# Kernel optimization log

Measured on AMD Instinct MI355X. Metric: run time of the kernel, lower is better.

The kernel has to match this reference:

```python
import jax, jax.numpy as jnp
import numpy as np

B, S, D, H, F = 8, 1024, 1024, 16, 4096
DH = D // H  # 64
EPS = 1e-5


def layer_norm(x, g, b):
    mu = jnp.mean(x, axis=-1, keepdims=True)
    var = jnp.mean(jnp.square(x - mu), axis=-1, keepdims=True)
    return (x - mu) * jax.lax.rsqrt(var + EPS) * g + b


def mha(q_in, k_in, v_in, wq, wk, wv, wo, causal):
    # wq/wk/wv: [H, D, DH] (stacked per-head nn.Linear weights, pre-transposed)
    Q = jnp.einsum('bsd,hdk->bhsk', q_in, wq)
    K = jnp.einsum('bsd,hdk->bhsk', k_in, wk)
    V = jnp.einsum('bsd,hdk->bhsk', v_in, wv)
    scores = jnp.einsum('bhsk,bhtk->bhst', Q, K) / jnp.sqrt(jnp.asarray(DH, Q.dtype))
    if causal:
        mask = jnp.triu(jnp.ones((S, S), dtype=bool), k=1)  # True = inaccessible
        scores = jnp.where(mask, -jnp.inf, scores)
    A = jax.nn.softmax(scores, axis=-1)
    heads = jnp.einsum('bhst,bhtk->bhsk', A, V)
    heads = heads.transpose(0, 2, 1, 3).reshape(q_in.shape[0], q_in.shape[1], D)
    return heads @ wo.T  # nn.Linear convention


def setup_inputs() -> dict:
    key = jax.random.key(0)
    ks = jax.random.split(key, 16)
    sc = 1.0 / np.sqrt(D)
    scf = 1.0 / np.sqrt(F)
    return {
        'embeds': jax.random.normal(ks[0], (B, S, D), jnp.float32),
        'encoder_output': jax.random.normal(ks[1], (B, S, D), jnp.float32),
        'wq1': jax.random.normal(ks[2], (H, D, DH), jnp.float32) * sc,
        'wk1': jax.random.normal(ks[3], (H, D, DH), jnp.float32) * sc,
        'wv1': jax.random.normal(ks[4], (H, D, DH), jnp.float32) * sc,
        'wo1': jax.random.normal(ks[5], (D, D), jnp.float32) * sc,
        'wq2': jax.random.normal(ks[6], (H, D, DH), jnp.float32) * sc,
        'wk2': jax.random.normal(ks[7], (H, D, DH), jnp.float32) * sc,
        'wv2': jax.random.normal(ks[8], (H, D, DH), jnp.float32) * sc,
        'wo2': jax.random.normal(ks[9], (D, D), jnp.float32) * sc,
        'ln1_g': jnp.ones((D,), jnp.float32), 'ln1_b': jnp.zeros((D,), jnp.float32),
        'ln2_g': jnp.ones((D,), jnp.float32), 'ln2_b': jnp.zeros((D,), jnp.float32),
        'ln3_g': jnp.ones((D,), jnp.float32), 'ln3_b': jnp.zeros((D,), jnp.float32),
        'w1': jax.random.normal(ks[10], (F, D), jnp.float32) * sc,
        'b1': jnp.zeros((F,), jnp.float32),
        'w2': jax.random.normal(ks[11], (D, F), jnp.float32) * scf,
        'b2': jnp.zeros((D,), jnp.float32),
    }


def reference(embeds, encoder_output, wq1, wk1, wv1, wo1, wq2, wk2, wv2, wo2,
              ln1_g, ln1_b, ln2_g, ln2_b, ln3_g, ln3_b, w1, b1, w2, b2):
    # masked (causal) self-attention + residual + LN
    sa = mha(embeds, embeds, embeds, wq1, wk1, wv1, wo1, causal=True)
    x1 = layer_norm(sa + embeds, ln1_g, ln1_b)
    # cross-attention (no mask) + residual + LN
    ca = mha(x1, encoder_output, encoder_output, wq2, wk2, wv2, wo2, causal=False)
    x2 = layer_norm(ca + x1, ln2_g, ln2_b)
    # feedforward (Linear -> GELU(exact) -> Linear) + residual + LN
    ff = jax.nn.gelu(x2 @ w1.T + b1, approximate=False) @ w2.T + b2
    return layer_norm(ff + x2, ln3_g, ln3_b)
```

## Files before the change

kernel.cpp:

```cpp
#include <hip/hip_runtime.h>
#include <cstdint>
#include <cstddef>

typedef unsigned short u16;
typedef __attribute__((ext_vector_type(4))) float f32x4;
typedef __attribute__((ext_vector_type(4))) float f4;
typedef __attribute__((ext_vector_type(8))) short short8x;
typedef __attribute__((ext_vector_type(4))) u16 u16x4;
typedef __attribute__((ext_vector_type(8))) u16 u16x8;

#define DEV static __device__ __forceinline__

DEV void gl_lds16(const void* g, void* l) {
  __builtin_amdgcn_global_load_lds(
      (const __attribute__((address_space(1))) unsigned int*)g,
      (__attribute__((address_space(3))) unsigned int*)l, 16, 0, 0);
}

DEV u16 f2bf(float f) {
  unsigned u = __float_as_uint(f);
  u += 0x7fffu + ((u >> 16) & 1u);
  return (u16)(u >> 16);
}


__global__ __launch_bounds__(256) void cast_bf16_2(const float* __restrict__ X0, const float* __restrict__ X1,
                                                   u16* __restrict__ Y0, u16* __restrict__ Y1) {
  const float* X = blockIdx.y ? X1 : X0;
  u16* Y = blockIdx.y ? Y1 : Y0;
  size_t i = ((size_t)blockIdx.x * 256 + threadIdx.x) * 4;
  f4 v = *(const f4*)(X + i);
  u16x4 y;
#pragma unroll
  for (int j = 0; j < 4; ++j) y[j] = f2bf(v[j]);
  *(u16x4*)(Y + i) = y;
}

__global__ __launch_bounds__(256) void cast_wqkv6(const float* __restrict__ W0, const float* __restrict__ W1,
                                                  const float* __restrict__ W2, const float* __restrict__ W3,
                                                  const float* __restrict__ W4, const float* __restrict__ W5,
                                                  u16* __restrict__ Wbase) {
  __shared__ float tile[64][65];
  const int t = threadIdx.x;
  const int h = blockIdx.y;
  const int z = blockIdx.z;
  const int d0 = blockIdx.x * 64;
  const float* W = (z == 0) ? W0 : (z == 1) ? W1 : (z == 2) ? W2 : (z == 3) ? W3 : (z == 4) ? W4 : W5;
  u16* Wt = Wbase + (size_t)z * (1024 * 1024);
  const float* Wb = W + (size_t)h * (1024 * 64);
  const int di = t >> 2;
  const int j0 = (t & 3) * 16;
#pragma unroll
  for (int c = 0; c < 4; ++c) {
    f4 v = *(const f4*)(Wb + (size_t)(d0 + di) * 64 + j0 + c * 4);
#pragma unroll
    for (int j = 0; j < 4; ++j) tile[di][j0 + c * 4 + j] = v[j];
  }
  __syncthreads();
  const int k = t >> 2;
  const int dd0 = (t & 3) * 16;
  u16x8 o0, o1;
#pragma unroll
  for (int u = 0; u < 8; ++u) o0[u] = f2bf(tile[dd0 + u][k]);
#pragma unroll
  for (int u = 0; u < 8; ++u) o1[u] = f2bf(tile[dd0 + 8 + u][k]);
  u16* dst = Wt + (size_t)(h * 64 + k) * 1024 + d0 + dd0;
  *(u16x8*)(dst) = o0;
  *(u16x8*)(dst + 8) = o1;
}

__global__ __launch_bounds__(256) void transpose_v(const u16* __restrict__ V, u16* __restrict__ Vt,
                                                   int vstride, int voff) {
  __shared__ u16 tile[32][72];
  const int t = threadIdx.x;
  const int bh = blockIdx.y;
  const int s0 = blockIdx.x * 32;
  const u16* Vb = V + (size_t)(bh >> 4) * (1024 * (size_t)vstride) + voff + (bh & 15) * 64;
  const int si = t >> 3, d0 = (t & 7) * 8;
  u16x8 val = *(const u16x8*)(Vb + (size_t)(s0 + si) * vstride + d0);
#pragma unroll
  for (int u = 0; u < 8; ++u) tile[si][d0 + u] = val[u];
  __syncthreads();
  const int d = t >> 2, sj0 = (t & 3) * 8;
  u16x8 o;
#pragma unroll
  for (int u = 0; u < 8; ++u) o[u] = tile[sj0 + u][d];
  *(u16x8*)(Vt + (size_t)bh * (64 * 1024) + (size_t)d * 1024 + s0 + sj0) = o;
}

template <int EPI>
__global__ __launch_bounds__(256, 3) void gemm_bt(const u16* __restrict__ A, const u16* __restrict__ Bt,
                                                  void* __restrict__ C, const float* __restrict__ bias,
                                                  int Krow, int Kit, int ldc, long long zC) {
  __shared__ u16 As0[128 * 32], Bs0[128 * 32];
  __shared__ u16 As1[128 * 32], Bs1[128 * 32];
  const int t = threadIdx.x;
  const int wave = t >> 6, lane = t & 63;
  const int lr = lane & 15, lkg = lane >> 4;
  const int swz = (lr >> 1) & 3;
  const int wr = (wave >> 1) * 64, wc = (wave & 1) * 64;

  const int gx = gridDim.x;
  const int nwg = gx * gridDim.y;
  const int flat = blockIdx.y * gx + blockIdx.x;
  const int wg = (flat & 7) * (nwg >> 3) + (flat >> 3);
  const int m0 = (wg / gx) * 128, n0 = (wg % gx) * 128;

  const int schunk = ((t & 3) ^ ((t >> 3) & 3)) << 4;
  const size_t rowb = (size_t)Krow * 2;
  const size_t rowskip = (size_t)64 * rowb;
  const size_t zoff = (size_t)blockIdx.z * (size_t)Kit * 2;
  const char* gA0 = (const char*)A + (size_t)(m0 + (t >> 2)) * rowb + zoff + schunk;
  const char* gA1 = gA0 + rowskip;
  const char* gB0 = (const char*)Bt + (size_t)(n0 + (t >> 2)) * rowb + zoff + schunk;
  const char* gB1 = gB0 + rowskip;

  char* dA0 = (char*)As0 + wave * 1024;
  char* dB0 = (char*)Bs0 + wave * 1024;
  char* dA1 = (char*)As1 + wave * 1024;
  char* dB1 = (char*)Bs1 + wave * 1024;

  const int aoff = (wr + lr) * 64 + ((lkg ^ swz) << 4);
  const int boff = (wc + lr) * 64 + ((lkg ^ swz) << 4);
  const char* rA0 = (const char*)As0 + aoff;
  const char* rB0 = (const char*)Bs0 + boff;
  const char* rA1 = (const char*)As1 + aoff;
  const char* rB1 = (const char*)Bs1 + boff;

  const f32x4 fzero = {0.f, 0.f, 0.f, 0.f};
  f32x4 acc[4][4];
#pragma unroll
  for (int m = 0; m < 4; ++m)
#pragma unroll
    for (int n = 0; n < 4; ++n) acc[m][n] = fzero;

  auto compute = [&](const char* rA, const char* rB) {
    short8x aF[4], bF[4];
#pragma unroll
    for (int m = 0; m < 4; ++m) aF[m] = *(const short8x*)(rA + m * 1024);
#pragma unroll
    for (int n = 0; n < 4; ++n) bF[n] = *(const short8x*)(rB + n * 1024);
#pragma unroll
    for (int m = 0; m < 4; ++m)
#pragma unroll
      for (int n = 0; n < 4; ++n)
        acc[m][n] = __builtin_amdgcn_mfma_f32_16x16x32_bf16(aF[m], bF[n], acc[m][n], 0, 0, 0);
  };

  gl_lds16(gA0, dA0); gl_lds16(gA1, dA0 + 4096);
  gl_lds16(gB0, dB0); gl_lds16(gB1, dB0 + 4096);
  gA0 += 64; gA1 += 64; gB0 += 64; gB1 += 64;
  __syncthreads();

  const int nk2 = Kit >> 6;
  for (int p = 0; p < nk2; ++p) {
    gl_lds16(gA0, dA1); gl_lds16(gA1, dA1 + 4096);
    gl_lds16(gB0, dB1); gl_lds16(gB1, dB1 + 4096);
    gA0 += 64; gA1 += 64; gB0 += 64; gB1 += 64;
    compute(rA0, rB0);
    __syncthreads();
    if (p + 1 < nk2) {
      gl_lds16(gA0, dA0); gl_lds16(gA1, dA0 + 4096);
      gl_lds16(gB0, dB0); gl_lds16(gB1, dB0 + 4096);
    }
    gA0 += 64; gA1 += 64; gB0 += 64; gB1 += 64;
    compute(rA1, rB1);
    __syncthreads();
  }

#pragma unroll
  for (int m = 0; m < 4; ++m) {
#pragma unroll
    for (int rr = 0; rr < 4; ++rr) {
      const int gm = m0 + wr + m * 16 + lkg * 4 + rr;
#pragma unroll
      for (int n = 0; n < 4; ++n) {
        const int gn = n0 + wc + n * 16 + lr;
        float v = acc[m][n][rr];
        if (EPI == 2) v += bias[gn];
        if (EPI == 2) v = 0.5f * v * (1.0f + erff(v * 0.70710678118654752f));
        if (EPI == 4) v *= 0.125f;
        if (EPI == 5 && gn < 1024) v *= 0.125f;
        if (EPI == 1)
          ((float*)C)[(size_t)blockIdx.z * zC + (size_t)gm * ldc + gn] = v;
        else
          ((u16*)C)[(size_t)gm * ldc + gn] = f2bf(v);
      }
    }
  }
}

__global__ __launch_bounds__(256, 3) void gemm_q2kv2(const u16* __restrict__ A1, const u16* __restrict__ B1,
                                                     u16* __restrict__ C1, const u16* __restrict__ A2,
                                                     const u16* __restrict__ B2, u16* __restrict__ C2) {
  __shared__ u16 As0[128 * 32], Bs0[128 * 32];
  __shared__ u16 As1[128 * 32], Bs1[128 * 32];
  const int t = threadIdx.x;
  const int wave = t >> 6, lane = t & 63;
  const int lr = lane & 15, lkg = lane >> 4;
  const int swz = (lr >> 1) & 3;
  const int wr = (wave >> 1) * 64, wc = (wave & 1) * 64;

  const int nwg = 24 * 64;
  const int flat = blockIdx.y * 24 + blockIdx.x;
  const int wg = (flat & 7) * (nwg >> 3) + (flat >> 3);

  const int sub = (wg >= 512);
  const int wl = sub ? (wg - 512) : wg;
  const int gxl = sub ? 16 : 8;
  const int m0 = (wl / gxl) * 128, n0 = (wl % gxl) * 128;
  const u16* A = sub ? A2 : A1;
  const u16* Bt = sub ? B2 : B1;
  u16* C = sub ? C2 : C1;
  const int ldc = sub ? 2048 : 3072;
  const float scale = sub ? 1.0f : 0.125f;

  const int schunk = ((t & 3) ^ ((t >> 3) & 3)) << 4;
  const size_t rowb = 2048;
  const size_t rowskip = (size_t)64 * rowb;
  const char* gA0 = (const char*)A + (size_t)(m0 + (t >> 2)) * rowb + schunk;
  const char* gA1 = gA0 + rowskip;
  const char* gB0 = (const char*)Bt + (size_t)(n0 + (t >> 2)) * rowb + schunk;
  const char* gB1 = gB0 + rowskip;

  char* dA0 = (char*)As0 + wave * 1024;
  char* dB0 = (char*)Bs0 + wave * 1024;
  char* dA1 = (char*)As1 + wave * 1024;
  char* dB1 = (char*)Bs1 + wave * 1024;

  const int aoff = (wr + lr) * 64 + ((lkg ^ swz) << 4);
  const int boff = (wc + lr) * 64 + ((lkg ^ swz) << 4);
  const char* rA0 = (const char*)As0 + aoff;
  const char* rB0 = (const char*)Bs0 + boff;
  const char* rA1 = (const char*)As1 + aoff;
  const char* rB1 = (const char*)Bs1 + boff;

  const f32x4 fzero = {0.f, 0.f, 0.f, 0.f};
  f32x4 acc[4][4];
#pragma unroll
  for (int m = 0; m < 4; ++m)
#pragma unroll
    for (int n = 0; n < 4; ++n) acc[m][n] = fzero;

  auto compute = [&](const char* rA, const char* rB) {
    short8x aF[4], bF[4];
#pragma unroll
    for (int m = 0; m < 4; ++m) aF[m] = *(const short8x*)(rA + m * 1024);
#pragma unroll
    for (int n = 0; n < 4; ++n) bF[n] = *(const short8x*)(rB + n * 1024);
#pragma unroll
    for (int m = 0; m < 4; ++m)
#pragma unroll
      for (int n = 0; n < 4; ++n)
        acc[m][n] = __builtin_amdgcn_mfma_f32_16x16x32_bf16(aF[m], bF[n], acc[m][n], 0, 0, 0);
  };

  gl_lds16(gA0, dA0); gl_lds16(gA1, dA0 + 4096);
  gl_lds16(gB0, dB0); gl_lds16(gB1, dB0 + 4096);
  gA0 += 64; gA1 += 64; gB0 += 64; gB1 += 64;
  __syncthreads();

  for (int p = 0; p < 16; ++p) {
    gl_lds16(gA0, dA1); gl_lds16(gA1, dA1 + 4096);
    gl_lds16(gB0, dB1); gl_lds16(gB1, dB1 + 4096);
    gA0 += 64; gA1 += 64; gB0 += 64; gB1 += 64;
    compute(rA0, rB0);
    __syncthreads();
    if (p + 1 < 16) {
      gl_lds16(gA0, dA0); gl_lds16(gA1, dA0 + 4096);
      gl_lds16(gB0, dB0); gl_lds16(gB1, dB0 + 4096);
    }
    gA0 += 64; gA1 += 64; gB0 += 64; gB1 += 64;
    compute(rA1, rB1);
    __syncthreads();
  }

#pragma unroll
  for (int m = 0; m < 4; ++m) {
#pragma unroll
    for (int rr = 0; rr < 4; ++rr) {
      const int gm = m0 + wr + m * 16 + lkg * 4 + rr;
#pragma unroll
      for (int n = 0; n < 4; ++n) {
        const int gn = n0 + wc + n * 16 + lr;
        C[(size_t)gm * ldc + gn] = f2bf(acc[m][n][rr] * scale);
      }
    }
  }
}

template <int CAUSAL>
__global__ __launch_bounds__(256, 2) void flash_attn(const u16* __restrict__ Q, const u16* __restrict__ Kk,
                                                     const u16* __restrict__ Vt, u16* __restrict__ O,
                                                     int qst, int kst) {
  __shared__ u16 Ks[2][64 * 64];
  __shared__ u16 Vs[2][64 * 64];
  __shared__ u16 Ps[4][32 * 72];
  const int t = threadIdx.x;
  const int wave = t >> 6, lane = t & 63;
  const int lr = lane & 15, lkg = lane >> 4, lk = lkg * 8;
  const int sw = lr & 7;
  const int bh = blockIdx.y;
  const u16* Qb = Q + (size_t)(bh >> 4) * (1024 * (size_t)qst) + (bh & 15) * 64;
  const u16* Kb = Kk + (size_t)(bh >> 4) * (1024 * (size_t)kst) + (bh & 15) * 64;
  const u16* Vtb = Vt + (size_t)bh * (64 * 1024);
  u16* Ob = O + (size_t)(bh >> 4) * (1024 * 1024) + (bh & 15) * 64;
  const int qt = (gridDim.x - 1 - blockIdx.x) * 128;
  const int qw = qt + wave * 32;

  const f32x4 fzero = {0.f, 0.f, 0.f, 0.f};
  short8x qf[2][2];
#pragma unroll
  for (int rb = 0; rb < 2; ++rb)
#pragma unroll
    for (int kk = 0; kk < 2; ++kk)
      qf[rb][kk] = *(const short8x*)(Qb + (size_t)(qw + rb * 16 + lr) * qst + kk * 32 + lk);

  float m_[2][4], l_[2][4];
  f32x4 o_[2][4];
#pragma unroll
  for (int rb = 0; rb < 2; ++rb) {
#pragma unroll
    for (int rr = 0; rr < 4; ++rr) { m_[rb][rr] = -1e30f; l_[rb][rr] = 0.f; }
#pragma unroll
    for (int db = 0; db < 4; ++db) o_[rb][db] = fzero;
  }

  const int rsel = lane >> 3;
  const int csw = ((lane & 7) ^ rsel) << 4;

  auto stage = [&](int buf, int kv0) {
#pragma unroll
    for (int s = 0; s < 2; ++s) {
      const int row = s * 32 + wave * 8 + rsel;
      gl_lds16((const char*)Kb + (size_t)(kv0 + row) * (size_t)(kst * 2) + csw,
               (char*)&Ks[buf][0] + s * 4096 + wave * 1024);
      gl_lds16((const char*)Vtb + (size_t)row * 2048 + (size_t)kv0 * 2 + csw,
               (char*)&Vs[buf][0] + s * 4096 + wave * 1024);
    }
  };

  const int kv_end = CAUSAL ? (qt + 128) : 1024;
  const int nt = kv_end >> 6;

  stage(0, 0);
  __syncthreads();
  int cur = 0;
  for (int tt = 0; tt < nt; ++tt) {
    const int kv0 = tt * 64;
    if (tt + 1 < nt) stage(cur ^ 1, kv0 + 64);

    const char* ksb = (const char*)&Ks[cur][0];
    const char* vsb = (const char*)&Vs[cur][0];

    short8x kf[4][2];
#pragma unroll
    for (int nb = 0; nb < 4; ++nb) {
      const int row = nb * 16 + lr;
#pragma unroll
      for (int kk = 0; kk < 2; ++kk)
        kf[nb][kk] = *(const short8x*)(ksb + row * 128 + (((kk * 4 + lkg) ^ sw) << 4));
    }

#pragma unroll
    for (int rb = 0; rb < 2; ++rb) {
      f32x4 s[4];
#pragma unroll
      for (int nb = 0; nb < 4; ++nb) {
        s[nb] = __builtin_amdgcn_mfma_f32_16x16x32_bf16(qf[rb][0], kf[nb][0], fzero, 0, 0, 0);
        s[nb] = __builtin_amdgcn_mfma_f32_16x16x32_bf16(qf[rb][1], kf[nb][1], s[nb], 0, 0, 0);
      }
      if (CAUSAL && (kv0 + 63 > qw + rb * 16)) {
#pragma unroll
        for (int rr = 0; rr < 4; ++rr) {
          const int qg = qw + rb * 16 + lkg * 4 + rr;
#pragma unroll
          for (int nb = 0; nb < 4; ++nb)
            if (kv0 + nb * 16 + lr > qg) s[nb][rr] = -1e30f;
        }
      }
#pragma unroll
      for (int rr = 0; rr < 4; ++rr) {
        float mx = fmaxf(fmaxf(s[0][rr], s[1][rr]), fmaxf(s[2][rr], s[3][rr]));
#pragma unroll
        for (int d = 1; d < 16; d <<= 1) mx = fmaxf(mx, __shfl_xor(mx, d, 16));
        const float mold = m_[rb][rr];
        const float mnew = fmaxf(mold, mx);
        float p[4];
#pragma unroll
        for (int nb = 0; nb < 4; ++nb) p[nb] = __expf(s[nb][rr] - mnew);
        float rsum = (p[0] + p[1]) + (p[2] + p[3]);
#pragma unroll
        for (int d = 1; d < 16; d <<= 1) rsum += __shfl_xor(rsum, d, 16);
        const float alpha = __expf(mold - mnew);
        m_[rb][rr] = mnew;
        l_[rb][rr] = l_[rb][rr] * alpha + rsum;
#pragma unroll
        for (int db = 0; db < 4; ++db) o_[rb][db][rr] *= alpha;
        const int prow = rb * 16 + lkg * 4 + rr;
#pragma unroll
        for (int nb = 0; nb < 4; ++nb)
          Ps[wave][prow * 72 + nb * 16 + lr] = f2bf(p[nb]);
      }
    }
    asm volatile("s_waitcnt lgkmcnt(0)" ::: "memory");

    short8x vF[4][2];
#pragma unroll
    for (int db = 0; db < 4; ++db) {
      const int row = db * 16 + lr;
#pragma unroll
      for (int kk = 0; kk < 2; ++kk)
        vF[db][kk] = *(const short8x*)(vsb + row * 128 + (((kk * 4 + lkg) ^ sw) << 4));
    }
#pragma unroll
    for (int rb = 0; rb < 2; ++rb) {
#pragma unroll
      for (int kk = 0; kk < 2; ++kk) {
        const short8x aP = *(const short8x*)((const char*)&Ps[wave][0] + (rb * 16 + lr) * 144 + kk * 64 + lkg * 16);
#pragma unroll
        for (int db = 0; db < 4; ++db)
          o_[rb][db] = __builtin_amdgcn_mfma_f32_16x16x32_bf16(aP, vF[db][kk], o_[rb][db], 0, 0, 0);
      }
    }
    __syncthreads();
    cur ^= 1;
  }

#pragma unroll
  for (int rb = 0; rb < 2; ++rb)
#pragma unroll
    for (int rr = 0; rr < 4; ++rr) {
      const float inv = 1.0f / l_[rb][rr];
      const int qg = qw + rb * 16 + lkg * 4 + rr;
#pragma unroll
      for (int db = 0; db < 4; ++db)
        Ob[(size_t)qg * 1024 + db * 16 + lr] = f2bf(o_[rb][db][rr] * inv);
    }
}

__global__ __launch_bounds__(256) void ln_res(const float* __restrict__ X, const float* __restrict__ X2,
                                              const float* __restrict__ bias, const float* __restrict__ R,
                                              const float* __restrict__ gam, const float* __restrict__ bet,
                                              float* __restrict__ oF, u16* __restrict__ oB) {
  __shared__ float red[8];
  const int row = blockIdx.x, t = threadIdx.x;
  const int wave = t >> 6, lane = t & 63;
  const size_t off = (size_t)row * 1024 + t * 4;
  f4 x = *(const f4*)(X + off);
  f4 r = *(const f4*)(R + off);
  float v[4];
#pragma unroll
  for (int j = 0; j < 4; ++j) v[j] = x[j] + r[j];
  if (X2) {
    f4 x2 = *(const f4*)(X2 + off);
#pragma unroll
    for (int j = 0; j < 4; ++j) v[j] += x2[j];
  }
  if (bias) {
    f4 bb = *(const f4*)(bias + t * 4);
#pragma unroll
    for (int j = 0; j < 4; ++j) v[j] += bb[j];
  }
  float s = 0.f, sq = 0.f;
#pragma unroll
  for (int j = 0; j < 4; ++j) { s += v[j]; sq += v[j] * v[j]; }
#pragma unroll
  for (int d = 1; d < 64; d <<= 1) {
    s += __shfl_xor(s, d, 64);
    sq += __shfl_xor(sq, d, 64);
  }
  if (lane == 0) { red[wave * 2] = s; red[wave * 2 + 1] = sq; }
  __syncthreads();
  s = red[0] + red[2] + red[4] + red[6];
  sq = red[1] + red[3] + red[5] + red[7];
  const float mu = s * (1.0f / 1024.0f);
  const float var = sq * (1.0f / 1024.0f) - mu * mu;
  const float rs = rsqrtf(var + 1e-5f);
  f4 g4 = *(const f4*)(gam + t * 4);
  f4 b4 = *(const f4*)(bet + t * 4);
  f4 y;
#pragma unroll
  for (int j = 0; j < 4; ++j) y[j] = (v[j] - mu) * rs * g4[j] + b4[j];
  *(f4*)(oF + off) = y;
  if (oB) {
    u16x4 yb;
#pragma unroll
    for (int j = 0; j < 4; ++j) yb[j] = f2bf(y[j]);
    *(u16x4*)(oB + off) = yb;
  }
}

extern "C" void kernel_launch(void* const* d_in, const int* in_sizes, int n_in,
                              void* d_out, int out_size, void* d_ws, size_t ws_size,
                              hipStream_t stream) {
  const float* embeds = (const float*)d_in[0];
  const float* enc = (const float*)d_in[1];
  const float* wq1 = (const float*)d_in[2];
  const float* wk1 = (const float*)d_in[3];
  const float* wv1 = (const float*)d_in[4];
  const float* wo1 = (const float*)d_in[5];
  const float* wq2 = (const float*)d_in[6];
  const float* wk2 = (const float*)d_in[7];
  const float* wv2 = (const float*)d_in[8];
  const float* wo2 = (const float*)d_in[9];
  const float* ln1g = (const float*)d_in[10];
  const float* ln1b = (const float*)d_in[11];
  const float* ln2g = (const float*)d_in[12];
  const float* ln2b = (const float*)d_in[13];
  const float* ln3g = (const float*)d_in[14];
  const float* ln3b = (const float*)d_in[15];
  const float* w1 = (const float*)d_in[16];
  const float* b1 = (const float*)d_in[17];
  const float* w2 = (const float*)d_in[18];
  const float* b2 = (const float*)d_in[19];
  float* out = (float*)d_out;
  char* ws = (char*)d_ws;
  const size_t MB = (size_t)1 << 20;

  u16* QKV = (u16*)(ws + 0 * MB);
  u16* Vtb = (u16*)(ws + 48 * MB);
  u16* Hd = (u16*)(ws + 64 * MB);
  float* Of = (float*)(ws + 80 * MB);
  u16* ebf = (u16*)(ws + 112 * MB);
  u16* encb = (u16*)(ws + 128 * MB);
  float* x1f = (float*)(ws + 144 * MB);
  float* x2f = (float*)(ws + 176 * MB);
  u16* Wq1t = (u16*)(ws + 208 * MB);
  u16* Wq2t = (u16*)(ws + 214 * MB);
  u16* Wk2t = (u16*)(ws + 216 * MB);
  u16* Wo1b = (u16*)(ws + 220 * MB);
  u16* Wo2b = (u16*)(ws + 222 * MB);
  u16* W1b = (u16*)(ws + 224 * MB);
  u16* W2b = (u16*)(ws + 232 * MB);
  u16* x1b = ebf;
  u16* x2b = encb;
  u16* Hff = (u16*)(ws + 0 * MB);

  u16* KV2 = (u16*)(ws + 176 * MB);
  float* P3 = (float*)(ws + 112 * MB);
  const long long ZC = (long long)8192 * 1024;

  dim3 blk(256);

  cast_bf16_2<<<dim3(8192, 2), blk, 0, stream>>>(embeds, enc, ebf, encb);
  cast_wqkv6<<<dim3(16, 16, 6), blk, 0, stream>>>(wq1, wk1, wv1, wq2, wk2, wv2, Wq1t);
  cast_bf16_2<<<dim3(1024, 2), blk, 0, stream>>>(wo1, wo2, Wo1b, Wo2b);
  cast_bf16_2<<<dim3(4096, 2), blk, 0, stream>>>(w1, w2, W1b, W2b);

  gemm_bt<5><<<dim3(24, 64), blk, 0, stream>>>(ebf, Wq1t, QKV, nullptr, 1024, 1024, 3072, 0);
  transpose_v<<<dim3(32, 128), blk, 0, stream>>>(QKV, Vtb, 3072, 2048);
  flash_attn<1><<<dim3(8, 128), blk, 0, stream>>>(QKV, QKV + 1024, Vtb, Hd, 3072, 3072);
  gemm_bt<1><<<dim3(8, 64), blk, 0, stream>>>(Hd, Wo1b, Of, nullptr, 1024, 1024, 1024, 0);
  ln_res<<<8192, blk, 0, stream>>>(Of, nullptr, nullptr, embeds, ln1g, ln1b, x1f, x1b);

  gemm_q2kv2<<<dim3(24, 64), blk, 0, stream>>>(x1b, Wq2t, QKV, encb, Wk2t, KV2);
  transpose_v<<<dim3(32, 128), blk, 0, stream>>>(KV2, Vtb, 2048, 1024);
  flash_attn<0><<<dim3(8, 128), blk, 0, stream>>>(QKV, KV2, Vtb, Hd, 3072, 2048);
  gemm_bt<1><<<dim3(8, 64), blk, 0, stream>>>(Hd, Wo2b, Of, nullptr, 1024, 1024, 1024, 0);
  ln_res<<<8192, blk, 0, stream>>>(Of, nullptr, nullptr, x1f, ln2g, ln2b, x2f, x2b);

  gemm_bt<2><<<dim3(32, 64), blk, 0, stream>>>(x2b, W1b, Hff, b1, 1024, 1024, 4096, 0);
  gemm_bt<1><<<dim3(8, 64, 2), blk, 0, stream>>>(Hff, W2b, Of, nullptr, 4096, 2048, 1024, ZC);
  ln_res<<<8192, blk, 0, stream>>>(Of, P3, b2, x2f, ln3g, ln3b, out, nullptr);
}
```

Measured before the change: 695.1 us.

## Triple-buffer GEMM LDS staging with vmcnt-based waits instead of full syncs

The bf16 GEMM moves from double buffering to a three-stage LDS ring, keeping two K-tiles of global-to-LDS loads in flight. Explicit s_waitcnt vmcnt(4) plus a single s_barrier per step replace the two __syncthreads per pair of tiles, so the next tile's loads overlap the current tile's MFMAs. The cost is 50% more LDS per block, which may reduce occupancy under launch_bounds(256,3). It also depends on hand-written waitcnt counts being correct, since the compiler does not track these asm waits.

```diff
diff --git a/kernel.cpp b/kernel.cpp
--- a/kernel.cpp
+++ b/kernel.cpp
@@ -10,6 +10,9 @@
 typedef __attribute__((ext_vector_type(8))) u16 u16x8;
 
 #define DEV static __device__ __forceinline__
+#define VMC4() asm volatile("s_waitcnt vmcnt(4)" ::: "memory")
+#define VMC0() asm volatile("s_waitcnt vmcnt(0)" ::: "memory")
+#define BARR() asm volatile("s_barrier" ::: "memory")
 
 DEV void gl_lds16(const void* g, void* l) {
   __builtin_amdgcn_global_load_lds(
@@ -94,6 +97,7 @@
                                                   int Krow, int Kit, int ldc, long long zC) {
   __shared__ u16 As0[128 * 32], Bs0[128 * 32];
   __shared__ u16 As1[128 * 32], Bs1[128 * 32];
+  __shared__ u16 As2[128 * 32], Bs2[128 * 32];
   const int t = threadIdx.x;
   const int wave = t >> 6, lane = t & 63;
   const int lr = lane & 15, lkg = lane >> 4;
@@ -115,17 +119,14 @@
   const char* gB0 = (const char*)Bt + (size_t)(n0 + (t >> 2)) * rowb + zoff + schunk;
   const char* gB1 = gB0 + rowskip;
 
-  char* dA0 = (char*)As0 + wave * 1024;
-  char* dB0 = (char*)Bs0 + wave * 1024;
-  char* dA1 = (char*)As1 + wave * 1024;
-  char* dB1 = (char*)Bs1 + wave * 1024;
-
   const int aoff = (wr + lr) * 64 + ((lkg ^ swz) << 4);
   const int boff = (wc + lr) * 64 + ((lkg ^ swz) << 4);
-  const char* rA0 = (const char*)As0 + aoff;
-  const char* rB0 = (const char*)Bs0 + boff;
-  const char* rA1 = (const char*)As1 + aoff;
-  const char* rB1 = (const char*)Bs1 + boff;
+  char* dA_c = (char*)As0 + wave * 1024;  char* dB_c = (char*)Bs0 + wave * 1024;
+  char* dA_n = (char*)As1 + wave * 1024;  char* dB_n = (char*)Bs1 + wave * 1024;
+  char* dA_t = (char*)As2 + wave * 1024;  char* dB_t = (char*)Bs2 + wave * 1024;
+  const char* rA_c = (const char*)As0 + aoff;  const char* rB_c = (const char*)Bs0 + boff;
+  const char* rA_n = (const char*)As1 + aoff;  const char* rB_n = (const char*)Bs1 + boff;
+  const char* rA_t = (const char*)As2 + aoff;  const char* rB_t = (const char*)Bs2 + boff;
 
   const f32x4 fzero = {0.f, 0.f, 0.f, 0.f};
   f32x4 acc[4][4];
@@ -134,6 +135,11 @@
 #pragma unroll
     for (int n = 0; n < 4; ++n) acc[m][n] = fzero;
 
+  auto stageTo = [&](char* da, char* db) {
+    gl_lds16(gA0, da); gl_lds16(gA1, da + 4096);
+    gl_lds16(gB0, db); gl_lds16(gB1, db + 4096);
+    gA0 += 64; gA1 += 64; gB0 += 64; gB1 += 64;
+  };
   auto compute = [&](const char* rA, const char* rB) {
     short8x aF[4], bF[4];
 #pragma unroll
@@ -147,25 +153,19 @@
         acc[m][n] = __builtin_amdgcn_mfma_f32_16x16x32_bf16(aF[m], bF[n], acc[m][n], 0, 0, 0);
   };
 
-  gl_lds16(gA0, dA0); gl_lds16(gA1, dA0 + 4096);
-  gl_lds16(gB0, dB0); gl_lds16(gB1, dB0 + 4096);
-  gA0 += 64; gA1 += 64; gB0 += 64; gB1 += 64;
-  __syncthreads();
-
-  const int nk2 = Kit >> 6;
-  for (int p = 0; p < nk2; ++p) {
-    gl_lds16(gA0, dA1); gl_lds16(gA1, dA1 + 4096);
-    gl_lds16(gB0, dB1); gl_lds16(gB1, dB1 + 4096);
-    gA0 += 64; gA1 += 64; gB0 += 64; gB1 += 64;
-    compute(rA0, rB0);
-    __syncthreads();
-    if (p + 1 < nk2) {
-      gl_lds16(gA0, dA0); gl_lds16(gA1, dA0 + 4096);
-      gl_lds16(gB0, dB0); gl_lds16(gB1, dB0 + 4096);
-    }
-    gA0 += 64; gA1 += 64; gB0 += 64; gB1 += 64;
-    compute(rA1, rB1);
-    __syncthreads();
+  const int nk = Kit >> 5;
+  stageTo(dA_c, dB_c);
+  stageTo(dA_n, dB_n);
+
+  for (int s = 0; s < nk; ++s) {
+    if (s + 1 < nk) { VMC4(); } else { VMC0(); }
+    BARR();
+    compute(rA_c, rB_c);
+    if (s + 2 < nk) stageTo(dA_t, dB_t);
+    char* ta = dA_c; dA_c = dA_n; dA_n = dA_t; dA_t = ta;
+    char* tb = dB_c; dB_c = dB_n; dB_n = dB_t; dB_t = tb;
+    const char* ra = rA_c; rA_c = rA_n; rA_n = rA_t; rA_t = ra;
+    const char* rb = rB_c; rB_c = rB_n; rB_n = rB_t; rB_t = rb;
   }
 
 #pragma unroll
```

Measured after the change: 715.3 us. +2.9%, slower.
